# Optimization experiments

Hardware: AMD Instinct MI355X
Metric: run time of the kernel (lower is better)

Reference implementation:

```python
import jax, jax.numpy as jnp
import numpy as np

B, S, N, D, C, H = 256, 256, 128, 256, 512, 4  # batch, seq, mem_slots, mem_dim, controller_dim, heads
HD = D // H


def setup_inputs() -> dict:
    key = jax.random.key(0)
    ks = jax.random.split(key, 12)
    sc = 0.02
    p = lambda k, shape: (jax.random.normal(k, shape, jnp.float32) * sc)
    return {
        "input_seq": jax.random.normal(ks[0], (B, S, D), jnp.float32),
        "memory_init": jax.random.normal(ks[1], (N, D), jnp.float32) * (np.sqrt(6.0 / (N + D)) / np.sqrt(3.0)),
        # LSTM (torch gate order i, f, g, o)
        "W_ih": p(ks[2], (4 * C, D)), "W_hh": p(ks[3], (4 * C, C)),
        "b_ih": jnp.zeros((4 * C,), jnp.float32), "b_hh": jnp.zeros((4 * C,), jnp.float32),
        # heads
        "W_read": p(ks[4], (D, C)), "b_read": jnp.zeros((D,), jnp.float32),
        "W_write": p(ks[5], (2 * D, C)), "b_write": jnp.zeros((2 * D,), jnp.float32),
        "W_erase": p(ks[6], (D, C)), "b_erase": jnp.zeros((D,), jnp.float32),
        # MultiheadAttention packed in-proj (q,k,v) + out-proj
        "W_in": p(ks[7], (3 * D, D)), "b_in": jnp.zeros((3 * D,), jnp.float32),
        "W_out": p(ks[8], (D, D)), "b_out": jnp.zeros((D,), jnp.float32),
        # gates
        "W_rg": p(ks[9], (1, C)), "b_rg": jnp.zeros((1,), jnp.float32),
        "W_wg": p(ks[10], (1, C)), "b_wg": jnp.zeros((1,), jnp.float32),
    }


def reference(input_seq, memory_init, W_ih, W_hh, b_ih, b_hh,
              W_read, b_read, W_write, b_write, W_erase, b_erase,
              W_in, b_in, W_out, b_out, W_rg, b_rg, W_wg, b_wg):
    b, s, d = input_seq.shape
    Wq, Wk, Wv = jnp.split(W_in, 3, axis=0)
    bq, bk, bv = jnp.split(b_in, 3)
    inv_sqrt_hd = 1.0 / np.sqrt(HD)

    mem0 = jnp.broadcast_to(memory_init, (b,) + memory_init.shape)
    h0 = jnp.zeros((b, C), input_seq.dtype)
    c0 = jnp.zeros((b, C), input_seq.dtype)

    def step(carry, x_t):
        h, c, mem = carry  # h,c: [B,C]; mem: [B,N,D]
        # LSTM cell (torch gate order i,f,g,o)
        gates = x_t @ W_ih.T + b_ih + h @ W_hh.T + b_hh
        i, f, g, o = jnp.split(gates, 4, axis=-1)
        c = jax.nn.sigmoid(f) * c + jax.nn.sigmoid(i) * jnp.tanh(g)
        h = jax.nn.sigmoid(o) * jnp.tanh(c)
        # --- read: MHA(query=read_key, key=value=memory) ---
        rk = h @ W_read.T + b_read                      # [B,D]
        q = (rk @ Wq.T + bq).reshape(b, H, HD)          # [B,H,hd]
        k = (mem @ Wk.T + bk).reshape(b, -1, H, HD)     # [B,N,H,hd]
        v = (mem @ Wv.T + bv).reshape(b, -1, H, HD)
        scores = jnp.einsum('bhd,bnhd->bhn', q, k) * inv_sqrt_hd
        attn = jax.nn.softmax(scores, axis=-1)          # [B,H,N]
        ctx = jnp.einsum('bhn,bnhd->bhd', attn, v).reshape(b, d)
        read_out = ctx @ W_out.T + b_out
        read_gate = jax.nn.sigmoid(h @ W_rg.T + b_rg)   # [B,1]
        read = read_gate * read_out
        # --- write: erase/add ---
        wp = h @ W_write.T + b_write
        write_key, write_val = wp[:, :d], wp[:, d:]
        erase_vec = jax.nn.sigmoid(h @ W_erase.T + b_erase)  # [B,D]
        write_gate = jax.nn.sigmoid(h @ W_wg.T + b_wg)       # [B,1]
        wa = jax.nn.softmax(jnp.einsum('bd,bnd->bn', write_key, mem), axis=-1)  # [B,N]
        ew = wa[:, :, None]                                   # [B,N,1]
        mem = mem * (1.0 - ew * erase_vec[:, None, :]) + write_gate[:, None, :] * (ew * write_val[:, None, :])
        return (h, c, mem), x_t + read

    (hT, cT, memT), outs = jax.lax.scan(step, (h0, c0, mem0), jnp.swapaxes(input_seq, 0, 1))
    output_sequence = jnp.swapaxes(outs, 0, 1)  # [B,S,D]
    return output_sequence, memT
```

## Files before the change

kernel.cpp:

```cpp
#include <hip/hip_runtime.h>

#define S_LEN 256
#define B_SZ  256
#define N_MEM 128
#define D_DIM 256
#define C_DIM 512
#define NBLK  256
#define MSTR  260
#define PROJS 1792
#define AGENT __HIP_MEMORY_SCOPE_AGENT

typedef __bf16 bf16x8 __attribute__((ext_vector_type(8)));
typedef unsigned short ushort4v __attribute__((ext_vector_type(4)));
typedef float floatx4 __attribute__((ext_vector_type(4)));
typedef float floatx2 __attribute__((ext_vector_type(2)));

__device__ __forceinline__ unsigned short f2bf(float f){
  unsigned u = __float_as_uint(f);
  u += 0x7FFFu + ((u >> 16) & 1u);
  return (unsigned short)(u >> 16);
}
__device__ __forceinline__ float bf2f(unsigned short v){
  return __uint_as_float(((unsigned)v) << 16);
}
__device__ __forceinline__ float sigm(float x){ return 1.f/(1.f + __expf(-x)); }
__device__ __forceinline__ floatx4 mfma16(bf16x8 a, bf16x8 b, floatx4 c){
  return __builtin_amdgcn_mfma_f32_16x16x32_bf16(a, b, c, 0, 0, 0);
}

__device__ __forceinline__ unsigned ald32(const void* p){
  return __hip_atomic_load((const unsigned*)p, __ATOMIC_RELAXED, AGENT);
}
__device__ __forceinline__ unsigned long long ald64(const void* p){
  return __hip_atomic_load((const unsigned long long*)p, __ATOMIC_RELAXED, AGENT);
}
__device__ __forceinline__ void ast32(void* p, unsigned v){
  __hip_atomic_store((unsigned*)p, v, __ATOMIC_RELAXED, AGENT);
}
__device__ __forceinline__ void ast64(void* p, unsigned long long v){
  __hip_atomic_store((unsigned long long*)p, v, __ATOMIC_RELAXED, AGENT);
}
__device__ __forceinline__ void sst16(void* p, unsigned short v){
  asm volatile("global_store_short %0, %1, off sc1" :: "v"(p), "v"(v) : "memory");
}

struct V16 { floatx4 v0,v1,v2,v3,v4,v5,v6,v7,v8,v9,v10,v11,v12,v13,v14,v15; };
#define BC(xx) __builtin_bit_cast(bf16x8, xx)

__device__ __forceinline__ V16 cload16(const unsigned short* base){
  V16 r;
  asm volatile(
    "global_load_dwordx4 %0, %16, off sc1\n\t"
    "global_load_dwordx4 %1, %16, off offset:64 sc1\n\t"
    "global_load_dwordx4 %2, %16, off offset:128 sc1\n\t"
    "global_load_dwordx4 %3, %16, off offset:192 sc1\n\t"
    "global_load_dwordx4 %4, %16, off offset:256 sc1\n\t"
    "global_load_dwordx4 %5, %16, off offset:320 sc1\n\t"
    "global_load_dwordx4 %6, %16, off offset:384 sc1\n\t"
    "global_load_dwordx4 %7, %16, off offset:448 sc1\n\t"
    "global_load_dwordx4 %8, %16, off offset:512 sc1\n\t"
    "global_load_dwordx4 %9, %16, off offset:576 sc1\n\t"
    "global_load_dwordx4 %10, %16, off offset:640 sc1\n\t"
    "global_load_dwordx4 %11, %16, off offset:704 sc1\n\t"
    "global_load_dwordx4 %12, %16, off offset:768 sc1\n\t"
    "global_load_dwordx4 %13, %16, off offset:832 sc1\n\t"
    "global_load_dwordx4 %14, %16, off offset:896 sc1\n\t"
    "global_load_dwordx4 %15, %16, off offset:960 sc1\n\t"
    "s_waitcnt vmcnt(0)"
    : "=&v"(r.v0), "=&v"(r.v1), "=&v"(r.v2), "=&v"(r.v3),
      "=&v"(r.v4), "=&v"(r.v5), "=&v"(r.v6), "=&v"(r.v7),
      "=&v"(r.v8), "=&v"(r.v9), "=&v"(r.v10), "=&v"(r.v11),
      "=&v"(r.v12), "=&v"(r.v13), "=&v"(r.v14), "=&v"(r.v15)
    : "v"(base)
    : "memory");
  __builtin_amdgcn_sched_barrier(0);
  return r;
}

__device__ __forceinline__ void cload16_issue(const unsigned short* base, floatx4 r[16]){
  asm volatile(
    "global_load_dwordx4 %0, %16, off sc1\n\t"
    "global_load_dwordx4 %1, %16, off offset:64 sc1\n\t"
    "global_load_dwordx4 %2, %16, off offset:128 sc1\n\t"
    "global_load_dwordx4 %3, %16, off offset:192 sc1\n\t"
    "global_load_dwordx4 %4, %16, off offset:256 sc1\n\t"
    "global_load_dwordx4 %5, %16, off offset:320 sc1\n\t"
    "global_load_dwordx4 %6, %16, off offset:384 sc1\n\t"
    "global_load_dwordx4 %7, %16, off offset:448 sc1\n\t"
    "global_load_dwordx4 %8, %16, off offset:512 sc1\n\t"
    "global_load_dwordx4 %9, %16, off offset:576 sc1\n\t"
    "global_load_dwordx4 %10, %16, off offset:640 sc1\n\t"
    "global_load_dwordx4 %11, %16, off offset:704 sc1\n\t"
    "global_load_dwordx4 %12, %16, off offset:768 sc1\n\t"
    "global_load_dwordx4 %13, %16, off offset:832 sc1\n\t"
    "global_load_dwordx4 %14, %16, off offset:896 sc1\n\t"
    "global_load_dwordx4 %15, %16, off offset:960 sc1"
    : "=&v"(r[0]), "=&v"(r[1]), "=&v"(r[2]), "=&v"(r[3]),
      "=&v"(r[4]), "=&v"(r[5]), "=&v"(r[6]), "=&v"(r[7]),
      "=&v"(r[8]), "=&v"(r[9]), "=&v"(r[10]), "=&v"(r[11]),
      "=&v"(r[12]), "=&v"(r[13]), "=&v"(r[14]), "=&v"(r[15])
    : "v"(base)
    : "memory");
}
__device__ __forceinline__ void cwait16(floatx4 r[16]){
  asm volatile("s_waitcnt vmcnt(0)"
    : "+v"(r[0]), "+v"(r[1]), "+v"(r[2]), "+v"(r[3]),
      "+v"(r[4]), "+v"(r[5]), "+v"(r[6]), "+v"(r[7]),
      "+v"(r[8]), "+v"(r[9]), "+v"(r[10]), "+v"(r[11]),
      "+v"(r[12]), "+v"(r[13]), "+v"(r[14]), "+v"(r[15])
    :: "memory");
  __builtin_amdgcn_sched_barrier(0);
}


__global__ __launch_bounds__(256) void p0_xbf(const float* __restrict__ x,
                                              unsigned short* __restrict__ xbf){
  int idx = (blockIdx.x*256 + threadIdx.x)*4;
  floatx4 f = *(const floatx4*)(x + idx);
  ushort4v u;
  u[0]=f2bf(f[0]); u[1]=f2bf(f[1]); u[2]=f2bf(f[2]); u[3]=f2bf(f[3]);
  *(ushort4v*)(xbf + idx) = u;
}

__global__ __launch_bounds__(256) void p1_wg(const float* __restrict__ Wih,
                                             const float* __restrict__ Whh,
                                             unsigned short* __restrict__ Wg){
  int idx = blockIdx.x*256 + threadIdx.x;
  int n = idx / 768, k = idx - n*768;
  float v = (k < 256) ? Wih[n*256 + k] : Whh[n*512 + (k-256)];
  Wg[idx] = f2bf(v);
}

__global__ __launch_bounds__(256) void p2_T(const float* __restrict__ Win,
                                            const float* __restrict__ Wread,
                                            const float* __restrict__ bread,
                                            const float* __restrict__ bin,
                                            float* __restrict__ T, float* __restrict__ rq){
  if (blockIdx.x < 512){
    int idx = blockIdx.x*256 + threadIdx.x;
    int e = idx >> 9, cc = idx & 511;
    float acc = 0.f;
    for (int dp = 0; dp < 256; ++dp) acc += Win[e*256 + dp] * Wread[dp*512 + cc];
    T[idx] = acc;
  } else {
    int e = threadIdx.x;
    float acc = bin[e];
    for (int dp = 0; dp < 256; ++dp) acc += bread[dp] * Win[e*256 + dp];
    rq[e] = acc;
  }
}

__global__ __launch_bounds__(256) void p3_w2(const float* __restrict__ Win,
                                             const float* __restrict__ Wwrite,
                                             const float* __restrict__ Werase,
                                             const float* __restrict__ Wrg,
                                             const float* __restrict__ Wwg,
                                             const float* __restrict__ bwrite,
                                             const float* __restrict__ berase,
                                             const float* __restrict__ brg,
                                             const float* __restrict__ bwg,
                                             const float* __restrict__ T,
                                             const float* __restrict__ rq,
                                             unsigned short* __restrict__ W2,
                                             float* __restrict__ bias2){
  int bid = blockIdx.x;
  if (bid < 2048){
    int idx = bid*256 + threadIdx.x;
    int j = idx >> 9, cc = idx & 511;
    int h = j >> 8, d = j & 255;
    float acc = 0.f;
    const float* wk = Win + (256 + h*64)*256 + d;
    const float* tp = T + (h*64)*512 + cc;
    for (int i = 0; i < 64; ++i) acc += wk[i*256] * tp[i*512];
    W2[(size_t)j*512 + cc] = f2bf(acc);
  } else if (bid < 2048 + 1568){
    int idx = (bid - 2048)*256 + threadIdx.x;
    int r = idx >> 9, cc = idx & 511;
    float v;
    if      (r < 512) v = Wwrite[r*512 + cc];
    else if (r < 768) v = Werase[(r-512)*512 + cc];
    else if (r == 768) v = Wrg[cc];
    else if (r == 769) v = Wwg[cc];
    else v = 0.f;
    W2[(size_t)(1024 + r)*512 + cc] = f2bf(v);
  } else {
    int j = (bid - 2048 - 1568)*256 + threadIdx.x;
    if (j >= 1808) return;
    float v;
    if (j < 1024){
      int h = j >> 8, d = j & 255;
      float acc = 0.f;
      for (int i = 0; i < 64; ++i) acc += rq[h*64+i] * Win[(256 + h*64 + i)*256 + d];
      v = acc;
    }
    else if (j < 1536) v = bwrite[j - 1024];
    else if (j < 1792) v = berase[j - 1536];
    else if (j == 1792) v = brg[0];
    else if (j == 1793) v = bwg[0];
    else v = 0.f;
    bias2[j] = v;
  }
}

__global__ __launch_bounds__(256) void p4_fold(const float* __restrict__ Win,
                                               const float* __restrict__ Wout,
                                               const float* __restrict__ bout,
                                               const float* __restrict__ bin,
                                               unsigned short* __restrict__ Fold,
                                               float* __restrict__ bout2){
  if (blockIdx.x < 1024){
    int idx = blockIdx.x*256 + threadIdx.x;
    int dp = idx >> 10, j = idx & 1023;
    int h = j & 3, d = j >> 2;
    float acc = 0.f;
    const float* wv = Win + (512 + h*64)*256 + d;
    const float* wo = Wout + dp*256 + h*64;
    for (int i = 0; i < 64; ++i) acc += wv[i*256] * wo[i];
    Fold[(size_t)dp*1024 + j] = f2bf(acc);
  } else {
    int dp = threadIdx.x;
    float acc = bout[dp];
    for (int e = 0; e < 256; ++e) acc += Wout[dp*256 + e] * bin[512 + e];
    bout2[dp] = acc;
  }
}

__global__ __launch_bounds__(256) void p5_init(const float* __restrict__ bih,
                                               const float* __restrict__ bhh,
                                               float* __restrict__ biasg,
                                               float* __restrict__ c,
                                               unsigned short* __restrict__ h0){
  int idx = blockIdx.x*256 + threadIdx.x;
  c[idx] = 0.f; h0[idx] = 0;
  if (idx < 2048) biasg[idx] = bih[idx] + bhh[idx];
}

__device__ __forceinline__ void gbarg(unsigned* cnt, unsigned target){
  __syncthreads();
  if (threadIdx.x == 0){
    __hip_atomic_fetch_add(cnt, 1u, __ATOMIC_RELAXED, AGENT);
    while (__hip_atomic_load(cnt, __ATOMIC_RELAXED, AGENT) < target)
      __builtin_amdgcn_s_sleep(1);
  }
  __builtin_amdgcn_sched_barrier(0);
  __syncthreads();
}


__device__ __forceinline__ void do_readout(int mt, int dt, int t,
                                           const unsigned short* __restrict__ mctx,
                                           const unsigned short* __restrict__ Fold,
                                           const float* __restrict__ rgb,
                                           const float* __restrict__ bout2,
                                           const float* __restrict__ x,
                                           float* __restrict__ out, int lane){
  const int lm = lane & 15, lk = (lane >> 4) * 8;
  const unsigned short* ap = mctx + (size_t)(mt*16 + lm)*1024 + lk;
  const unsigned short* bp = Fold + (size_t)(dt*16 + lm)*1024 + lk;
  const int r0 = mt*16 + ((lane >> 4) << 2);
  const float rg0 = __uint_as_float(ald32(&rgb[r0]));
  const float rg1 = __uint_as_float(ald32(&rgb[r0+1]));
  const float rg2 = __uint_as_float(ald32(&rgb[r0+2]));
  const float rg3 = __uint_as_float(ald32(&rgb[r0+3]));
  V16 a0 = cload16(ap);
  V16 a1 = cload16(ap + 512);
  const bf16x8 av[16] = {BC(a0.v0),BC(a0.v1),BC(a0.v2),BC(a0.v3),BC(a0.v4),BC(a0.v5),BC(a0.v6),BC(a0.v7),
                         BC(a0.v8),BC(a0.v9),BC(a0.v10),BC(a0.v11),BC(a0.v12),BC(a0.v13),BC(a0.v14),BC(a0.v15)};
  const bf16x8 bv[16] = {BC(a1.v0),BC(a1.v1),BC(a1.v2),BC(a1.v3),BC(a1.v4),BC(a1.v5),BC(a1.v6),BC(a1.v7),
                         BC(a1.v8),BC(a1.v9),BC(a1.v10),BC(a1.v11),BC(a1.v12),BC(a1.v13),BC(a1.v14),BC(a1.v15)};
  floatx4 acc = {0,0,0,0};
  #pragma unroll
  for (int kt = 0; kt < 16; ++kt)
    acc = mfma16(av[kt], *(const bf16x8*)(bp + kt*32), acc);
  #pragma unroll
  for (int kt = 0; kt < 16; ++kt)
    acc = mfma16(bv[kt], *(const bf16x8*)(bp + 512 + kt*32), acc);
  const int dp = dt*16 + lm;
  const float bo = bout2[dp];
  const float rg[4] = {rg0, rg1, rg2, rg3};
  #pragma unroll
  for (int q = 0; q < 4; ++q){
    const int bb = r0 + q;
    const size_t oi = ((size_t)bb * S_LEN + (t-1)) * D_DIM + dp;
    out[oi] = x[oi] + rg[q] * (acc[q] + bo);
  }
}

__global__ __launch_bounds__(512) void kmain(
    const float* __restrict__ x,
    const unsigned short* __restrict__ xbf,
    const unsigned short* __restrict__ Wg,
    const float* __restrict__ biasg,
    const unsigned short* __restrict__ W2, const float* __restrict__ bias2,
    const unsigned short* __restrict__ Fold, const float* __restrict__ bout2,
    float* __restrict__ cbuf,
    unsigned short* __restrict__ h0buf, unsigned short* __restrict__ h1buf,
    unsigned short* __restrict__ projB, unsigned short* __restrict__ mctx,
    float* __restrict__ rgbuf, const float* __restrict__ mem0,
    float* __restrict__ memT, float* __restrict__ out,
    unsigned* __restrict__ barcnt)
{
  const int bid = blockIdx.x, tid = threadIdx.x;
  const int lane = tid & 63, wave = tid >> 6;
  const int lm = lane & 15, lk = (lane >> 4) * 8;

  __shared__ float memL[128][MSTR];
  __shared__ float scU[5][512];
  __shared__ float qkW[5][256];
  __shared__ float er[256];
  __shared__ float wvs[256];
  __shared__ float attT[128][8];
  __shared__ float hL[512];
  __shared__ float wgS;
  float (*ga)[16][32] = (float (*)[16][32])&scU[0][0];

  const int r = bid >> 4, uc = bid & 15, u0 = uc*32;
  unsigned* gcnt = barcnt + r*16;

  for (int i = tid; i < 32768; i += 512) memL[i >> 8][i & 255] = mem0[i];

  unsigned nbar = 0;
  const unsigned short* hr = h0buf;
  unsigned short* hw = h1buf;
  const int g = wave >> 1, colh = wave & 1;
  const int row = r*16 + lm;
  const int slot = uc*8 + wave;

  floatx4 hq[16];
  bf16x8 xfr[8];
  cload16_issue(hr + (size_t)row*C_DIM + lk, hq);
  {
    const unsigned short* ax = xbf + ((size_t)row*S_LEN + 0)*D_DIM + lk;
    #pragma unroll
    for (int kt = 0; kt < 8; ++kt) xfr[kt] = *(const bf16x8*)(ax + kt*32);
  }

  for (int t = 0; t < S_LEN; ++t){
    {
      const unsigned short* wb = Wg + (size_t)(g*512 + u0 + colh*16 + lm)*768 + lk;
      cwait16(hq);
      floatx4 acc = {0,0,0,0};
      #pragma unroll
      for (int kt = 0; kt < 8; ++kt)
        acc = mfma16(xfr[kt], *(const bf16x8*)(wb + kt*32), acc);
      #pragma unroll
      for (int kt = 0; kt < 16; ++kt)
        acc = mfma16(BC(hq[kt]), *(const bf16x8*)(wb + 256 + kt*32), acc);
      const int rr0 = (lane >> 4) << 2;
      #pragma unroll
      for (int q = 0; q < 4; ++q) ga[g][rr0+q][colh*16 + lm] = acc[q];
      __syncthreads();
      if (tid < 256){
        const int ri = tid >> 4, cp = (tid & 15) * 2;
        const int b = r*16 + ri, u = u0 + cp;
        floatx2 bg0 = *(const floatx2*)&biasg[u];
        floatx2 bg1 = *(const floatx2*)&biasg[512 + u];
        floatx2 bg2 = *(const floatx2*)&biasg[1024 + u];
        floatx2 bg3 = *(const floatx2*)&biasg[1536 + u];
        const float gi0 = ga[0][ri][cp]   + bg0[0];
        const float gf0 = ga[1][ri][cp]   + bg1[0];
        const float gg0 = ga[2][ri][cp]   + bg2[0];
        const float go0 = ga[3][ri][cp]   + bg3[0];
        const float gi1 = ga[0][ri][cp+1] + bg0[1];
        const float gf1 = ga[1][ri][cp+1] + bg1[1];
        const float gg1 = ga[2][ri][cp+1] + bg2[1];
        const float go1 = ga[3][ri][cp+1] + bg3[1];
        const int ci2 = b*512 + u;
        floatx2 cv = *(const floatx2*)&cbuf[ci2];
        const float cn0 = sigm(gf0) * cv[0] + sigm(gi0) * tanhf(gg0);
        const float cn1 = sigm(gf1) * cv[1] + sigm(gi1) * tanhf(gg1);
        floatx2 cw; cw[0] = cn0; cw[1] = cn1;
        *(floatx2*)&cbuf[ci2] = cw;
        const unsigned hv2 = (unsigned)f2bf(sigm(go0) * tanhf(cn0))
                           | ((unsigned)f2bf(sigm(go1) * tanhf(cn1)) << 16);
        ast32((unsigned*)hw + (ci2 >> 1), hv2);
      }
    }
    gbarg(gcnt, (++nbar)*16u);
    {
      if (slot < 112){
        const int nt = slot;
        const unsigned short* ap = hw + (size_t)(r*16 + lm)*512 + lk;
        const unsigned short* bp = W2 + (size_t)(nt*16 + lm)*512 + lk;
        V16 av16 = cload16(ap);
        const bf16x8 av[16] = {BC(av16.v0),BC(av16.v1),BC(av16.v2),BC(av16.v3),BC(av16.v4),BC(av16.v5),BC(av16.v6),BC(av16.v7),
                               BC(av16.v8),BC(av16.v9),BC(av16.v10),BC(av16.v11),BC(av16.v12),BC(av16.v13),BC(av16.v14),BC(av16.v15)};
        floatx4 acc = {0,0,0,0};
        #pragma unroll
        for (int kt = 0; kt < 16; ++kt)
          acc = mfma16(av[kt], *(const bf16x8*)(bp + kt*32), acc);
        const int r0 = r*16 + ((lane >> 4) << 2);
        const int cc = nt*16 + lm;
        const float bv = bias2[cc];
        const bool sg = (cc >= 1536);
        #pragma unroll
        for (int q = 0; q < 4; ++q){
          float v = acc[q] + bv;
          if (sg) v = sigm(v);
          sst16(&projB[(size_t)(r0 + q)*PROJS + cc], f2bf(v));
        }
      } else if (t >= 1){
        do_readout(r, slot - 112, t, mctx, Fold, rgbuf, bout2, x, out, lane);
      }
    }
    gbarg(gcnt, (++nbar)*16u);
    {
      const unsigned long long* p64 = (const unsigned long long*)(projB + (size_t)bid*PROJS);
      if (tid < 448){
        unsigned long long u2 = ald64(p64 + tid);
        float e0 = bf2f((unsigned short)(u2 & 0xFFFFu));
        float e1 = bf2f((unsigned short)((u2 >> 16) & 0xFFFFu));
        float e2 = bf2f((unsigned short)((u2 >> 32) & 0xFFFFu));
        float e3 = bf2f((unsigned short)(u2 >> 48));
        const int j = tid*4;
        if (j < 1024){ float* q = &qkW[j>>8][j&255]; q[0]=e0; q[1]=e1; q[2]=e2; q[3]=e3; }
        else if (j < 1280){ float* q = &qkW[4][j-1024]; q[0]=e0; q[1]=e1; q[2]=e2; q[3]=e3; }
        else if (j < 1536){ float* q = &wvs[j-1280]; q[0]=e0; q[1]=e1; q[2]=e2; q[3]=e3; }
        else { float* q = &er[j-1536]; q[0]=e0; q[1]=e1; q[2]=e2; q[3]=e3; }
      } else {
        const int i = tid - 448;
        const unsigned long long* h64 = (const unsigned long long*)(hw + (size_t)bid*C_DIM);
        unsigned long long a = ald64(h64 + 2*i), b = ald64(h64 + 2*i + 1);
        float* q = &hL[i*8];
        q[0]=bf2f((unsigned short)(a & 0xFFFFu)); q[1]=bf2f((unsigned short)((a>>16)&0xFFFFu));
        q[2]=bf2f((unsigned short)((a>>32)&0xFFFFu)); q[3]=bf2f((unsigned short)(a>>48));
        q[4]=bf2f((unsigned short)(b & 0xFFFFu)); q[5]=bf2f((unsigned short)((b>>16)&0xFFFFu));
        q[6]=bf2f((unsigned short)((b>>32)&0xFFFFu)); q[7]=bf2f((unsigned short)(b>>48));
      }
      __syncthreads();
      if (wave >= 6){
        const int rowW = 1792 + (wave - 6);
        const unsigned short* wrow = W2 + (size_t)rowW*512 + lane*8;
        const float* hp = &hL[lane*8];
        float s = 0.f;
        #pragma unroll
        for (int c = 0; c < 8; ++c) s += hp[c] * bf2f(wrow[c]);
        #pragma unroll
        for (int off = 32; off; off >>= 1) s += __shfl_xor(s, off);
        if (lane == 0){
          const float v = sigm(s + bias2[rowW]);
          if (wave == 6) ast32(&rgbuf[bid], __float_as_uint(v));
          else wgS = v;
        }
      }
      {
        const int n = tid & 127, quarter = tid >> 7, db = quarter*64;
        const float* mr = &memL[n][db];
        floatx4 A0={0,0,0,0},A1={0,0,0,0},A2={0,0,0,0},A3={0,0,0,0},A4={0,0,0,0};
        #pragma unroll 4
        for (int i = 0; i < 64; i += 4){
          floatx4 m4 = *(const floatx4*)(mr + i);
          floatx4 q0 = *(const floatx4*)&qkW[0][db+i];
          floatx4 q1 = *(const floatx4*)&qkW[1][db+i];
          floatx4 q2 = *(const floatx4*)&qkW[2][db+i];
          floatx4 q3 = *(const floatx4*)&qkW[3][db+i];
          floatx4 qw = *(const floatx4*)&qkW[4][db+i];
          A0 += m4*q0; A1 += m4*q1; A2 += m4*q2; A3 += m4*q3; A4 += m4*qw;
        }
        scU[0][tid] = A0[0]+A0[1]+A0[2]+A0[3];
        scU[1][tid] = A1[0]+A1[1]+A1[2]+A1[3];
        scU[2][tid] = A2[0]+A2[1]+A2[2]+A2[3];
        scU[3][tid] = A3[0]+A3[1]+A3[2]+A3[3];
        scU[4][tid] = A4[0]+A4[1]+A4[2]+A4[3];
      }
      __syncthreads();
      if (tid < 128){
        #pragma unroll
        for (int j = 0; j < 5; ++j){
          float v = scU[j][tid] + scU[j][tid+128] + scU[j][tid+256] + scU[j][tid+384];
          scU[j][tid] = (j < 4) ? v * 0.125f : v;
        }
      }
      __syncthreads();
      {
        const int w = tid >> 6, l = tid & 63;
        if (w < 5){
          const int j = w;
          float v0 = scU[j][l], v1 = scU[j][l + 64];
          float mx = fmaxf(v0, v1);
          #pragma unroll
          for (int off = 32; off; off >>= 1) mx = fmaxf(mx, __shfl_xor(mx, off));
          float e0 = __expf(v0 - mx), e1 = __expf(v1 - mx);
          float sm = e0 + e1;
          #pragma unroll
          for (int off = 32; off; off >>= 1) sm += __shfl_xor(sm, off);
          float inv = 1.f / sm;
          attT[l][j] = e0 * inv; attT[l + 64][j] = e1 * inv;
        }
      }
      __syncthreads();
      {
        const float wgv = wgS;
        const int dlow = lane & 7, ng = lane >> 3;
        const int d4 = (wave*8 + dlow)*4;
        floatx4 er4 = *(const floatx4*)&er[d4];
        floatx4 wv4 = *(const floatx4*)&wvs[d4];
        floatx4 A0={0,0,0,0},A1={0,0,0,0},A2={0,0,0,0},A3={0,0,0,0};
        #pragma unroll 4
        for (int k = 0; k < 16; ++k){
          const int n = ng + k*8;
          floatx4 m = *(const floatx4*)&memL[n][d4];
          floatx4 a4 = *(const floatx4*)&attT[n][0];
          const float aw = attT[n][4];
          A0 += a4[0]*m; A1 += a4[1]*m; A2 += a4[2]*m; A3 += a4[3]*m;
          m = m * (1.f - aw*er4) + (wgv*aw) * wv4;
          *(floatx4*)&memL[n][d4] = m;
        }
        #pragma unroll
        for (int off = 8; off <= 32; off <<= 1){
          #pragma unroll
          for (int c = 0; c < 4; ++c){
            A0[c] += __shfl_xor(A0[c], off);
            A1[c] += __shfl_xor(A1[c], off);
            A2[c] += __shfl_xor(A2[c], off);
            A3[c] += __shfl_xor(A3[c], off);
          }
        }
        if (ng == 0){
          unsigned long long* mrow = (unsigned long long*)(mctx + (size_t)bid*1024);
          #pragma unroll
          for (int dd = 0; dd < 4; ++dd){
            const unsigned lo = (unsigned)f2bf(A0[dd]) | ((unsigned)f2bf(A1[dd]) << 16);
            const unsigned hi = (unsigned)f2bf(A2[dd]) | ((unsigned)f2bf(A3[dd]) << 16);
            ast64(mrow + d4 + dd, (unsigned long long)lo | ((unsigned long long)hi << 32));
          }
        }
      }
      {
        const int tn = (t+1 < S_LEN) ? t+1 : t;
        const unsigned short* ax = xbf + ((size_t)row*S_LEN + tn)*D_DIM + lk;
        #pragma unroll
        for (int kt = 0; kt < 8; ++kt) xfr[kt] = *(const bf16x8*)(ax + kt*32);
        cload16_issue(hw + (size_t)row*C_DIM + lk, hq);
      }
    }
    unsigned short* tmp = (unsigned short*)hr; hr = hw; hw = tmp;
  }
  gbarg(gcnt, (++nbar)*16u);
  if (wave == 0)
    do_readout(r, uc, S_LEN, mctx, Fold, rgbuf, bout2, x, out, lane);
  for (int i = tid; i < 32768; i += 512)
    memT[(size_t)bid * 32768 + i] = memL[i >> 8][i & 255];
}


extern "C" void kernel_launch(void* const* d_in, const int* in_sizes, int n_in,
                              void* d_out, int out_size, void* d_ws, size_t ws_size,
                              hipStream_t stream){
  const float* x      = (const float*)d_in[0];
  const float* mem0   = (const float*)d_in[1];
  const float* Wih    = (const float*)d_in[2];
  const float* Whh    = (const float*)d_in[3];
  const float* bih    = (const float*)d_in[4];
  const float* bhh    = (const float*)d_in[5];
  const float* Wread  = (const float*)d_in[6];
  const float* bread  = (const float*)d_in[7];
  const float* Wwrite = (const float*)d_in[8];
  const float* bwrite = (const float*)d_in[9];
  const float* Werase = (const float*)d_in[10];
  const float* berase = (const float*)d_in[11];
  const float* Win    = (const float*)d_in[12];
  const float* bin    = (const float*)d_in[13];
  const float* Wout   = (const float*)d_in[14];
  const float* bout   = (const float*)d_in[15];
  const float* Wrg    = (const float*)d_in[16];
  const float* brg    = (const float*)d_in[17];
  const float* Wwg    = (const float*)d_in[18];
  const float* bwg    = (const float*)d_in[19];
  float* out = (float*)d_out;
  float* memT = out + (size_t)B_SZ * S_LEN * D_DIM;

  char* ws = (char*)d_ws;
  size_t off = 0;
  auto alloc = [&](size_t bytes) -> void* {
    void* p = ws + off; off += (bytes + 511) & ~(size_t)511; return p;
  };
  unsigned short* xbf  = (unsigned short*)alloc((size_t)B_SZ*S_LEN*D_DIM*2);
  unsigned short* Wg   = (unsigned short*)alloc((size_t)2048*768*2);
  unsigned short* W2   = (unsigned short*)alloc((size_t)1808*512*2);
  unsigned short* Fold = (unsigned short*)alloc((size_t)256*1024*2);
  float* T     = (float*)alloc((size_t)256*512*4);
  float* rq    = (float*)alloc(256*4);
  float* bias2 = (float*)alloc(1808*4);
  float* bout2 = (float*)alloc(256*4);
  float* biasg = (float*)alloc(2048*4);
  float* cbuf  = (float*)alloc((size_t)256*512*4);
  unsigned short* h0 = (unsigned short*)alloc((size_t)256*512*2);
  unsigned short* h1 = (unsigned short*)alloc((size_t)256*512*2);
  unsigned short* projB = (unsigned short*)alloc((size_t)256*PROJS*2);
  unsigned short* mctx = (unsigned short*)alloc((size_t)256*1024*2);
  float* rgbuf = (float*)alloc(256*4);
  unsigned* barcnt = (unsigned*)alloc(4096);
  (void)ws_size; (void)in_sizes; (void)n_in; (void)out_size;

  (void)hipMemsetAsync(barcnt, 0, 4096, stream);
  p0_xbf <<<16384, 256, 0, stream>>>(x, xbf);
  p1_wg  <<<6144, 256, 0, stream>>>(Wih, Whh, Wg);
  p2_T   <<<513,  256, 0, stream>>>(Win, Wread, bread, bin, T, rq);
  p3_w2  <<<3624, 256, 0, stream>>>(Win, Wwrite, Werase, Wrg, Wwg, bwrite, berase, brg, bwg, T, rq, W2, bias2);
  p4_fold<<<1025, 256, 0, stream>>>(Win, Wout, bout, bin, Fold, bout2);
  p5_init<<<512,  256, 0, stream>>>(bih, bhh, biasg, cbuf, h0);

  kmain<<<NBLK, 512, 0, stream>>>(x, xbf, Wg, biasg, W2, bias2, Fold, bout2,
                                  cbuf, h0, h1, projB, mctx, rgbuf, mem0, memT, out, barcnt);
}
```

Before: 8.960 ms.

## Replace padded LDS memory layout with XOR-swizzle and hoist next-step prefetch

Replaces the padded [128][260] LDS memory buffer with an unpadded 32768-float array addressed through an XOR swizzle of the 16-byte column block by the slot index. Both the score loop and the erase/add/context loop use the swizzled addresses, with the aim of avoiding bank conflicts without padding. The prefetch of the next timestep's x fragments and h loads is also moved ahead of the memory update loop so it overlaps with that work. The risks are extra address arithmetic and higher register pressure from the earlier prefetch.

```diff
diff --git a/kernel.cpp b/kernel.cpp
--- a/kernel.cpp
+++ b/kernel.cpp
@@ -6,7 +6,6 @@
 #define D_DIM 256
 #define C_DIM 512
 #define NBLK  256
-#define MSTR  260
 #define PROJS 1792
 #define AGENT __HIP_MEMORY_SCOPE_AGENT
 
@@ -26,6 +25,10 @@
 __device__ __forceinline__ float sigm(float x){ return 1.f/(1.f + __expf(-x)); }
 __device__ __forceinline__ floatx4 mfma16(bf16x8 a, bf16x8 b, floatx4 c){
   return __builtin_amdgcn_mfma_f32_16x16x32_bf16(a, b, c, 0, 0, 0);
+}
+
+__device__ __forceinline__ int msw(int n, int d){
+  return (n << 8) + ((((d >> 2) ^ (n & 7)) << 2) | (d & 3));
 }
 
 __device__ __forceinline__ unsigned ald32(const void* p){
@@ -304,7 +307,7 @@
   const int lane = tid & 63, wave = tid >> 6;
   const int lm = lane & 15, lk = (lane >> 4) * 8;
 
-  __shared__ float memL[128][MSTR];
+  __shared__ float memF[32768];
   __shared__ float scU[5][512];
   __shared__ float qkW[5][256];
   __shared__ float er[256];
@@ -317,7 +320,10 @@
   const int r = bid >> 4, uc = bid & 15, u0 = uc*32;
   unsigned* gcnt = barcnt + r*16;
 
-  for (int i = tid; i < 32768; i += 512) memL[i >> 8][i & 255] = mem0[i];
+  for (int i = tid; i < 32768; i += 512){
+    const int n = i >> 8, d = i & 255;
+    memF[msw(n, d)] = mem0[i];
+  }
 
   unsigned nbar = 0;
   const unsigned short* hr = h0buf;
@@ -445,11 +451,12 @@
       }
       {
         const int n = tid & 127, quarter = tid >> 7, db = quarter*64;
-        const float* mr = &memL[n][db];
+        const int c7 = n & 7;
+        const float* mrow = &memF[n << 8];
         floatx4 A0={0,0,0,0},A1={0,0,0,0},A2={0,0,0,0},A3={0,0,0,0},A4={0,0,0,0};
         #pragma unroll 4
         for (int i = 0; i < 64; i += 4){
-          floatx4 m4 = *(const floatx4*)(mr + i);
+          floatx4 m4 = *(const floatx4*)(mrow + ((((db+i)>>2) ^ c7) << 2));
           floatx4 q0 = *(const floatx4*)&qkW[0][db+i];
           floatx4 q1 = *(const floatx4*)&qkW[1][db+i];
           floatx4 q2 = *(const floatx4*)&qkW[2][db+i];
@@ -490,21 +497,31 @@
       }
       __syncthreads();
       {
+        const int tn = (t+1 < S_LEN) ? t+1 : t;
+        const unsigned short* ax = xbf + ((size_t)row*S_LEN + tn)*D_DIM + lk;
+        #pragma unroll
+        for (int kt = 0; kt < 8; ++kt) xfr[kt] = *(const bf16x8*)(ax + kt*32);
+        cload16_issue(hw + (size_t)row*C_DIM + lk, hq);
+      }
+      {
         const float wgv = wgS;
         const int dlow = lane & 7, ng = lane >> 3;
-        const int d4 = (wave*8 + dlow)*4;
+        const int dblk = wave*8 + dlow;
+        const int pblk = dblk ^ ng;
+        const int d4 = dblk*4;
         floatx4 er4 = *(const floatx4*)&er[d4];
         floatx4 wv4 = *(const floatx4*)&wvs[d4];
         floatx4 A0={0,0,0,0},A1={0,0,0,0},A2={0,0,0,0},A3={0,0,0,0};
         #pragma unroll 4
         for (int k = 0; k < 16; ++k){
           const int n = ng + k*8;
-          floatx4 m = *(const floatx4*)&memL[n][d4];
+          float* maddr = &memF[(n << 8) + (pblk << 2)];
+          floatx4 m = *(const floatx4*)maddr;
           floatx4 a4 = *(const floatx4*)&attT[n][0];
           const float aw = attT[n][4];
           A0 += a4[0]*m; A1 += a4[1]*m; A2 += a4[2]*m; A3 += a4[3]*m;
           m = m * (1.f - aw*er4) + (wgv*aw) * wv4;
-          *(floatx4*)&memL[n][d4] = m;
+          *(floatx4*)maddr = m;
         }
         #pragma unroll
         for (int off = 8; off <= 32; off <<= 1){
@@ -517,21 +534,14 @@
           }
         }
         if (ng == 0){
-          unsigned long long* mrow = (unsigned long long*)(mctx + (size_t)bid*1024);
+          unsigned long long* mrow2 = (unsigned long long*)(mctx + (size_t)bid*1024);
           #pragma unroll
           for (int dd = 0; dd < 4; ++dd){
             const unsigned lo = (unsigned)f2bf(A0[dd]) | ((unsigned)f2bf(A1[dd]) << 16);
             const unsigned hi = (unsigned)f2bf(A2[dd]) | ((unsigned)f2bf(A3[dd]) << 16);
-            ast64(mrow + d4 + dd, (unsigned long long)lo | ((unsigned long long)hi << 32));
+            ast64(mrow2 + d4 + dd, (unsigned long long)lo | ((unsigned long long)hi << 32));
           }
         }
-      }
-      {
-        const int tn = (t+1 < S_LEN) ? t+1 : t;
-        const unsigned short* ax = xbf + ((size_t)row*S_LEN + tn)*D_DIM + lk;
-        #pragma unroll
-        for (int kt = 0; kt < 8; ++kt) xfr[kt] = *(const bf16x8*)(ax + kt*32);
-        cload16_issue(hw + (size_t)row*C_DIM + lk, hq);
       }
     }
     unsigned short* tmp = (unsigned short*)hr; hr = hw; hw = tmp;
@@ -539,8 +549,10 @@
   gbarg(gcnt, (++nbar)*16u);
   if (wave == 0)
     do_readout(r, uc, S_LEN, mctx, Fold, rgbuf, bout2, x, out, lane);
-  for (int i = tid; i < 32768; i += 512)
-    memT[(size_t)bid * 32768 + i] = memL[i >> 8][i & 255];
+  for (int i = tid; i < 32768; i += 512){
+    const int n = i >> 8, d = i & 255;
+    memT[(size_t)bid * 32768 + i] = memF[msw(n, d)];
+  }
 }
 
 
```

Result: no change. 9.081 ms (+1.4%).
